# Performance work log

Hardware: AMD Instinct MI355X
Metric: run time of the kernel (lower is better)

## Reference

```python
import jax, jax.numpy as jnp
import numpy as np

INV_GRID_SCALING = 1.0 / 1.48
LRELU_SLOPE = 0.2  # LReLULayer = Linear + leaky_relu(0.2)

N_GRIDS = 64
N_FEATS = 2
GRID_RES = 64
NODES = 128
N_OUT = 1
N_PTS = 1048576


def trilinear_sample(grid, coords):
    """torch.nn.functional.grid_sample, 3D bilinear (trilinear), align_corners=True,
    padding_mode='zeros'. grid: [C, D, H, W]; coords: [N, 3] normalized (x,y,z) in [-1,1]
    where x indexes W, y indexes H, z indexes D. Returns [C, N]."""
    C, D, H, W = grid.shape
    fx = (coords[:, 0] + 1.0) * 0.5 * (W - 1)
    fy = (coords[:, 1] + 1.0) * 0.5 * (H - 1)
    fz = (coords[:, 2] + 1.0) * 0.5 * (D - 1)
    x0 = jnp.floor(fx); y0 = jnp.floor(fy); z0 = jnp.floor(fz)
    wx = fx - x0; wy = fy - y0; wz = fz - z0
    x0 = x0.astype(jnp.int32); y0 = y0.astype(jnp.int32); z0 = z0.astype(jnp.int32)
    x1 = x0 + 1; y1 = y0 + 1; z1 = z0 + 1

    def gather(zi, yi, xi):
        valid = ((zi >= 0) & (zi < D) & (yi >= 0) & (yi < H) & (xi >= 0) & (xi < W))
        zc = jnp.clip(zi, 0, D - 1)
        yc = jnp.clip(yi, 0, H - 1)
        xc = jnp.clip(xi, 0, W - 1)
        return grid[:, zc, yc, xc] * valid.astype(grid.dtype)[None, :]  # [C, N]

    c000 = gather(z0, y0, x0); c001 = gather(z0, y0, x1)
    c010 = gather(z0, y1, x0); c011 = gather(z0, y1, x1)
    c100 = gather(z1, y0, x0); c101 = gather(z1, y0, x1)
    c110 = gather(z1, y1, x0); c111 = gather(z1, y1, x1)

    c00 = c000 * (1 - wx) + c001 * wx
    c01 = c010 * (1 - wx) + c011 * wx
    c10 = c100 * (1 - wx) + c101 * wx
    c11 = c110 * (1 - wx) + c111 * wx
    c0 = c00 * (1 - wy) + c01 * wy
    c1 = c10 * (1 - wy) + c11 * wy
    return c0 * (1 - wz) + c1 * wz  # [C, N]


def amgsrn_forward(x, grid_scales, grid_translations, feature_grids,
                   W0, b0, W1, b1, W2, b2):
    G, C = feature_grids.shape[0], feature_grids.shape[1]
    N = x.shape[0]
    # Per-grid affine transform: [G, N, 3]
    coords = (x[None, :, :] * grid_scales[:, None, :]
              + grid_translations[:, None, :]) * INV_GRID_SCALING
    coords = jax.lax.stop_gradient(coords)  # torch detaches grid_sample coords
    # Multi-grid trilinear lookup: [G, C, N]
    feats = jax.vmap(trilinear_sample)(feature_grids, coords)
    # flatten(0,1).permute(1,0) -> [N, G*C]
    feats = feats.reshape(G * C, N).T
    # Decoder: LReLU(128) -> LReLU(128) -> Linear(1)
    h = jax.nn.leaky_relu(feats @ W0.T + b0, LRELU_SLOPE)
    h = jax.nn.leaky_relu(h @ W1.T + b1, LRELU_SLOPE)
    return h @ W2.T + b2


def setup_inputs() -> dict:
    key = jax.random.key(0)
    ks = jax.random.split(key, 10)
    x = jax.random.uniform(ks[0], (N_PTS, 3), jnp.float32, -1.0, 1.0)
    grid_scales = jax.random.uniform(ks[1], (N_GRIDS, 3), jnp.float32, 1.0, 1.25) * 1.48
    grid_translations = jax.random.uniform(ks[2], (N_GRIDS, 3), jnp.float32, -1.0, 1.0) * (grid_scales - 1.0)
    feature_grids = jax.random.uniform(ks[3], (N_GRIDS, N_FEATS, GRID_RES, GRID_RES, GRID_RES),
                                       jnp.float32, -1e-4, 1e-4)
    d_in = N_GRIDS * N_FEATS
    W0 = jax.random.normal(ks[4], (NODES, d_in), jnp.float32) * (2.0 / (d_in + NODES)) ** 0.5
    b0 = jax.random.normal(ks[5], (NODES,), jnp.float32) * 0.001
    W1 = jax.random.normal(ks[6], (NODES, NODES), jnp.float32) * (2.0 / (2 * NODES)) ** 0.5
    b1 = jax.random.normal(ks[7], (NODES,), jnp.float32) * 0.001
    W2 = jax.random.normal(ks[8], (N_OUT, NODES), jnp.float32) * (2.0 / (NODES + N_OUT)) ** 0.5
    b2 = jax.random.normal(ks[9], (N_OUT,), jnp.float32) * 0.001
    return {"x": x, "grid_scales": grid_scales, "grid_translations": grid_translations,
            "feature_grids": feature_grids, "W0": W0, "b0": b0,
            "W1": W1, "b1": b1, "W2": W2, "b2": b2}


def reference(x, grid_scales, grid_translations, feature_grids, W0, b0, W1, b1, W2, b2):
    return amgsrn_forward(x, grid_scales, grid_translations, feature_grids,
                          W0, b0, W1, b1, W2, b2)
```

## Files before the change

### kernel.cpp

```cpp
#include <hip/hip_runtime.h>

#define NG 64
#define RES 64
#define RES3 (RES*RES*RES)
#define NODES 128
#define NBINS 262144
#define FBLOCK 512
#define LDS_PITCH 132

#define PDIM 67
#define PZSTR 4489
#define PGSTR 300763
#define PFOLD 4557

typedef short    short8 __attribute__((ext_vector_type(8)));
typedef float    f32x16 __attribute__((ext_vector_type(16)));
typedef float    f32x4  __attribute__((ext_vector_type(4)));
typedef unsigned uint4v __attribute__((ext_vector_type(4)));

__device__ __forceinline__ float lrelu(float v) { return fmaxf(v, 0.2f * v); }

__device__ __forceinline__ unsigned cvtpk(float lo, float hi) {
    unsigned r;
    asm("v_cvt_pk_bf16_f32 %0, %1, %2" : "=v"(r) : "v"(lo), "v"(hi));
    return r;
}
__device__ __forceinline__ float lo16f(unsigned u) { return __uint_as_float(u << 16); }
__device__ __forceinline__ float hi16f(unsigned u) { return __uint_as_float(u & 0xffff0000u); }

__device__ __forceinline__ void swap32(unsigned &x, unsigned &y) {
    auto rr = __builtin_amdgcn_permlane32_swap(x, y, false, false);
    x = rr[0]; y = rr[1];
}

__device__ __forceinline__ int bin_of(float x, float y, float z) {
    int bx = min(max((int)((x + 1.0f) * 32.0f), 0), 63);
    int by = min(max((int)((y + 1.0f) * 32.0f), 0), 63);
    int bz = min(max((int)((z + 1.0f) * 32.0f), 0), 63);
    return (bz << 12) | (by << 6) | bx;
}

__device__ __forceinline__ int xcd_swz(int bid, int nblocks) {
    const int q = nblocks >> 3, r = nblocks & 7;
    const int xcd = bid & 7, idx = bid >> 3;
    return (xcd < r ? xcd * (q + 1) : r * (q + 1) + (xcd - r) * q) + idx;
}

__global__ void hist_k(const float* __restrict__ xs, unsigned* __restrict__ cnt, int npts) {
    int n = blockIdx.x * blockDim.x + threadIdx.x;
    if (n >= npts) return;
    atomicAdd(&cnt[bin_of(xs[n*3], xs[n*3+1], xs[n*3+2])], 1u);
}

__global__ void scan1_k(const unsigned* __restrict__ cnt, unsigned* __restrict__ offs,
                        unsigned* __restrict__ bsum) {
    __shared__ unsigned wsum[4];
    const int t = threadIdx.x, lane = t & 63, wid = t >> 6;
    const int base = blockIdx.x * 1024 + t * 4;
    const uint4v v = *(const uint4v*)(cnt + base);
    const unsigned run = v.x + v.y + v.z + v.w;
    unsigned inc = run;
    #pragma unroll
    for (int d = 1; d < 64; d <<= 1) {
        const unsigned u = __shfl_up(inc, d);
        if (lane >= d) inc += u;
    }
    if (lane == 63) wsum[wid] = inc;
    __syncthreads();
    unsigned wbase = 0;
    #pragma unroll
    for (int i = 0; i < 4; ++i) wbase += (i < wid) ? wsum[i] : 0u;
    const unsigned pre = wbase + inc - run;
    uint4v o;
    o.x = pre; o.y = o.x + v.x; o.z = o.y + v.y; o.w = o.z + v.z;
    *(uint4v*)(offs + base) = o;
    if (t == 255) bsum[blockIdx.x] = wbase + inc;
}

__global__ void scan2_k(const unsigned* __restrict__ bsum, unsigned* __restrict__ bbase) {
    __shared__ unsigned wsum[4];
    const int t = threadIdx.x, lane = t & 63, wid = t >> 6;
    const unsigned v = bsum[t];
    unsigned inc = v;
    #pragma unroll
    for (int d = 1; d < 64; d <<= 1) {
        const unsigned u = __shfl_up(inc, d);
        if (lane >= d) inc += u;
    }
    if (lane == 63) wsum[wid] = inc;
    __syncthreads();
    unsigned wbase = 0;
    #pragma unroll
    for (int i = 0; i < 4; ++i) wbase += (i < wid) ? wsum[i] : 0u;
    bbase[t] = wbase + inc - v;
}

__global__ void scan3_k(unsigned* __restrict__ offs, const unsigned* __restrict__ bbase) {
    const unsigned add = bbase[blockIdx.x];
    uint4v* o4 = (uint4v*)(offs) + blockIdx.x * 256 + threadIdx.x;
    uint4v v = *o4;
    v.x += add; v.y += add; v.z += add; v.w += add;
    *o4 = v;
}

__global__ void scatter_k(const float* __restrict__ xs, unsigned* __restrict__ offs,
                          float4* __restrict__ sp, int npts) {
    int n = blockIdx.x * blockDim.x + threadIdx.x;
    if (n >= npts) return;
    float x = xs[n*3], y = xs[n*3+1], z = xs[n*3+2];
    unsigned p = atomicAdd(&offs[bin_of(x, y, z)], 1u);
    sp[p] = make_float4(x, y, z, __int_as_float(n));
}

__global__ __launch_bounds__(256, 8)
void repack_pad_k(const float* __restrict__ g, float2* __restrict__ wg) {
    const int gz = blockIdx.x;
    const int gi = gz / PDIM;
    const int zp = gz - gi * PDIM;
    const float* base = g + ((size_t)gi << 19);
    float2* dst = wg + (size_t)gi * PGSTR + (size_t)zp * PZSTR;
    const int zr = zp - 1;
    const bool zok = (unsigned)zr < 64u;
    const int w    = threadIdx.x >> 6;
    const int lane = threadIdx.x & 63;
    for (int yp = w; yp < PDIM; yp += 4) {
        const int yr = yp - 1;
        const bool rowok = zok && (unsigned)yr < 64u;
        float2 v = make_float2(0.0f, 0.0f);
        if (rowok) {
            const int o = (zr * 64 + yr) * 64 + lane;
            v.x = base[o]; v.y = base[o + RES3];
        }
        float2* drow = dst + yp * PDIM;
        drow[1 + lane] = v;
        if (lane < 3) drow[lane == 0 ? 0 : 64 + lane] = make_float2(0.0f, 0.0f);
    }
}

__global__ void packw_k(const float* __restrict__ W0, const float* __restrict__ W1,
                        const float* __restrict__ b0, const float* __restrict__ b1,
                        const float* __restrict__ W2,
                        const float* __restrict__ scales, const float* __restrict__ trans,
                        unsigned* __restrict__ wp0, unsigned* __restrict__ wp1,
                        float* __restrict__ b0p, float* __restrict__ b1p, float* __restrict__ w2p,
                        float4* __restrict__ coefA, float4* __restrict__ coefB)
{
    const int i = blockIdx.x * 256 + threadIdx.x;
    if (i < 8192) {
        const int q = i & 3, l = (i >> 2) & 63, s = (i >> 8) & 7, jt = i >> 11;
        const int j  = jt * 32 + (l & 31);
        const int k0 = s * 16 + (l >> 5) * 8 + q * 2;
        wp0[i] = cvtpk(W0[j*128 + k0], W0[j*128 + k0 + 1]);
        wp1[i] = cvtpk(W1[j*128 + k0], W1[j*128 + k0 + 1]);
    } else if (i < 8320) {
        const int t = i - 8192;
        const int r = t & 15, h = (t >> 4) & 1, jt = t >> 5;
        const int f = 32*jt + (r & 3) + 8*(r >> 2) + 4*h;
        b0p[t] = b0[f]; b1p[t] = b1[f]; w2p[t] = W2[f];
    } else if (i < 8384) {
        const int g = i - 8320;
        constexpr float K = 31.5f / 1.48f;
        coefA[g] = make_float4(scales[g*3+0]*K, scales[g*3+1]*K, scales[g*3+2]*K, 0.0f);
        coefB[g] = make_float4(fmaf(trans[g*3+0], K, 31.5f),
                               fmaf(trans[g*3+1], K, 31.5f),
                               fmaf(trans[g*3+2], K, 31.5f), 0.0f);
    }
}

__global__ __launch_bounds__(256, 8)
void gather_k(const float4* __restrict__ sp,
              const float2* __restrict__ gpad,
              const float4* __restrict__ coefA,
              const float4* __restrict__ coefB,
              uint4v* __restrict__ feats4,
              int npts, int npad, int nblocks)
{
    const int bid  = xcd_swz(blockIdx.x, nblocks);
    const int sidx = bid * 256 + threadIdx.x;
    const float4 P = sp[min(sidx, npts - 1)];
    const float px = P.x, py = P.y, pz = P.z;
    const char* gb = (const char*)gpad;

    #pragma unroll 2
    for (int g4 = 0; g4 < 16; ++g4) {
        unsigned fw[4];
        #pragma unroll
        for (int q = 0; q < 4; ++q) {
            const int g = g4 * 4 + q;
            const float4 cA = coefA[g];
            const float4 cB = coefB[g];
            float fx = fmaf(px, cA.x, cB.x);
            float fy = fmaf(py, cA.y, cB.y);
            float fz = fmaf(pz, cA.z, cB.z);
            fx = fminf(fmaxf(fx, -1.0f), 64.0f);
            fy = fminf(fmaxf(fy, -1.0f), 64.0f);
            fz = fminf(fmaxf(fz, -1.0f), 64.0f);
            const float fx0 = floorf(fx), fy0 = floorf(fy), fz0 = floorf(fz);
            const float wx = fx - fx0, wy = fy - fy0, wz = fz - fz0;
            const int x0 = (int)fx0, y0 = (int)fy0, z0 = (int)fz0;

            const int cell = g * PGSTR + z0 * PZSTR + y0 * PDIM + x0 + PFOLD;
            const char* p = gb + (unsigned)cell * 8u;
            const f32x4 A00 = *(const f32x4*)(p);
            const f32x4 A01 = *(const f32x4*)(p + (unsigned)(PDIM*8));
            const f32x4 A10 = *(const f32x4*)(p + (unsigned)(PZSTR*8));
            const f32x4 A11 = *(const f32x4*)(p + (unsigned)((PZSTR+PDIM)*8));

            const float wx0 = 1.0f - wx, wy0 = 1.0f - wy, wz0 = 1.0f - wz;
            const float w00 = wz0*wy0, w01 = wz0*wy, w10 = wz*wy0, w11 = wz*wy;

            const float f0 = w00*fmaf(wx, A00.z, wx0*A00.x)
                           + w01*fmaf(wx, A01.z, wx0*A01.x)
                           + w10*fmaf(wx, A10.z, wx0*A10.x)
                           + w11*fmaf(wx, A11.z, wx0*A11.x);
            const float f1 = w00*fmaf(wx, A00.w, wx0*A00.y)
                           + w01*fmaf(wx, A01.w, wx0*A01.y)
                           + w10*fmaf(wx, A10.w, wx0*A10.y)
                           + w11*fmaf(wx, A11.w, wx0*A11.y);
            fw[q] = cvtpk(f0, f1);
        }
        __builtin_nontemporal_store((uint4v){fw[0], fw[1], fw[2], fw[3]},
                                    &feats4[(size_t)g4 * npad + sidx]);
    }
}

__global__ __launch_bounds__(512, 4)
void mlp_k(const float4* __restrict__ sp,
           const uint4v* __restrict__ feats4,
           const uint4v* __restrict__ wp0,
           const uint4v* __restrict__ wp1,
           const float*  __restrict__ b0p,
           const float*  __restrict__ b1p,
           const float*  __restrict__ w2p,
           const float*  __restrict__ b2,
           float* __restrict__ out, int npts, int npad)
{
    __shared__ uint4v sW0[2048];
    __shared__ uint4v sW1[2048];

    const int tid = threadIdx.x;
    #pragma unroll
    for (int i = 0; i < 4; ++i) {
        sW0[tid + 512*i] = wp0[tid + 512*i];
        sW1[tid + 512*i] = wp1[tid + 512*i];
    }

    const int w   = tid >> 6;
    const int l   = tid & 63;
    const int p31 = l & 31;
    const int h   = l >> 5;

    const int pidx = blockIdx.x * 256 + w * 32 + p31;

    f32x16 acc[4];
    #pragma unroll
    for (int jt = 0; jt < 4; ++jt)
        #pragma unroll
        for (int q4 = 0; q4 < 4; ++q4) {
            const float4 bv = *reinterpret_cast<const float4*>(b0p + jt*32 + h*16 + q4*4);
            acc[jt][q4*4+0] = bv.x; acc[jt][q4*4+1] = bv.y;
            acc[jt][q4*4+2] = bv.z; acc[jt][q4*4+3] = bv.w;
        }

    __syncthreads();

    #pragma unroll
    for (int s = 0; s < 8; ++s) {
        const uint4v fw = __builtin_nontemporal_load(&feats4[(size_t)(2*s + h) * npad + pidx]);
        const short8 bfr = __builtin_bit_cast(short8, fw);
        #pragma unroll
        for (int jt = 0; jt < 4; ++jt) {
            const short8 wa = __builtin_bit_cast(short8, sW0[(jt*8 + s)*64 + l]);
            acc[jt] = __builtin_amdgcn_mfma_f32_32x32x16_bf16(wa, bfr, acc[jt], 0, 0, 0);
        }
    }

    float psum = 0.0f;
    #pragma unroll
    for (int jt2 = 0; jt2 < 4; ++jt2) {
        f32x16 a2;
        #pragma unroll
        for (int q4 = 0; q4 < 4; ++q4) {
            const float4 bv = *reinterpret_cast<const float4*>(b1p + jt2*32 + h*16 + q4*4);
            a2[q4*4+0] = bv.x; a2[q4*4+1] = bv.y;
            a2[q4*4+2] = bv.z; a2[q4*4+3] = bv.w;
        }
        #pragma unroll
        for (int s = 0; s < 8; ++s) {
            const int jt    = s >> 1;
            const int rbase = (s & 1) * 4;
            unsigned hw[4], rw[4];
            #pragma unroll
            for (int i = 0; i < 4; ++i) {
                const int rp = rbase + i;
                float v0 = acc[jt][2*rp],  v1 = acc[jt][2*rp+1];
                v0 = fmaxf(v0, 0.2f*v0);   v1 = fmaxf(v1, 0.2f*v1);
                hw[i] = cvtpk(v0, v1);
                rw[i] = cvtpk(v0 - lo16f(hw[i]), v1 - hi16f(hw[i]));
            }
            swap32(hw[0], hw[2]); swap32(hw[1], hw[3]);
            swap32(rw[0], rw[2]); swap32(rw[1], rw[3]);

            const short8 wa = __builtin_bit_cast(short8, sW1[(jt2*8 + s)*64 + l]);
            const short8 bh = __builtin_bit_cast(short8, (uint4v){hw[0], hw[1], hw[2], hw[3]});
            const short8 br = __builtin_bit_cast(short8, (uint4v){rw[0], rw[1], rw[2], rw[3]});
            a2 = __builtin_amdgcn_mfma_f32_32x32x16_bf16(wa, bh, a2, 0, 0, 0);
            a2 = __builtin_amdgcn_mfma_f32_32x32x16_bf16(wa, br, a2, 0, 0, 0);
        }
        #pragma unroll
        for (int q4 = 0; q4 < 4; ++q4) {
            const float4 wv = *reinterpret_cast<const float4*>(w2p + jt2*32 + h*16 + q4*4);
            const float* wc = (const float*)&wv;
            #pragma unroll
            for (int c = 0; c < 4; ++c) {
                float h1 = a2[q4*4+c];
                h1 = fmaxf(h1, 0.2f*h1);
                psum = fmaf(h1, wc[c], psum);
            }
        }
    }
    const float tot = psum + __shfl_xor(psum, 32);
    if (h == 0 && pidx < npts) {
        const float ow = ((const float*)sp)[4*pidx + 3];
        out[__float_as_int(ow)] = tot + b2[0];
    }
}

__global__ __launch_bounds__(256, 3)
void fused_k(const float4* __restrict__ sp,
             const float2* __restrict__ gpad,
             const float4* __restrict__ coefA,
             const float4* __restrict__ coefB,
             const uint4v* __restrict__ wp0,
             const uint4v* __restrict__ wp1,
             const float*  __restrict__ b0p,
             const float*  __restrict__ b1p,
             const float*  __restrict__ w2p,
             const float*  __restrict__ b2,
             float* __restrict__ out, int npts, int nblocks)
{
    const int bid = xcd_swz(blockIdx.x, nblocks);
    const int tid = threadIdx.x;
    const int w   = tid >> 6;
    const int l   = tid & 63;
    const int p31 = l & 31;
    const int h   = l >> 5;
    const int h4  = h * 4;

    const int pidx = bid * 128 + w * 32 + p31;
    const float4 P = sp[min(pidx, npts - 1)];
    const float px = P.x, py = P.y, pz = P.z;

    f32x16 acc[4];
    #pragma unroll
    for (int jt = 0; jt < 4; ++jt)
        #pragma unroll
        for (int q4 = 0; q4 < 4; ++q4) {
            const float4 bv = *reinterpret_cast<const float4*>(b0p + jt*32 + h*16 + q4*4);
            acc[jt][q4*4+0] = bv.x; acc[jt][q4*4+1] = bv.y;
            acc[jt][q4*4+2] = bv.z; acc[jt][q4*4+3] = bv.w;
        }

    const char* gb = (const char*)gpad;

    #pragma unroll 1
    for (int s = 0; s < 8; ++s) {
        unsigned fr[4];
        #pragma unroll
        for (int gi = 0; gi < 4; ++gi) {
            const int g = s*8 + h4 + gi;
            const float4 cA = coefA[g];
            const float4 cB = coefB[g];
            float fx = fmaf(px, cA.x, cB.x);
            float fy = fmaf(py, cA.y, cB.y);
            float fz = fmaf(pz, cA.z, cB.z);
            fx = fminf(fmaxf(fx, -1.0f), 64.0f);
            fy = fminf(fmaxf(fy, -1.0f), 64.0f);
            fz = fminf(fmaxf(fz, -1.0f), 64.0f);
            const float fx0 = floorf(fx), fy0 = floorf(fy), fz0 = floorf(fz);
            const float wx = fx - fx0, wy = fy - fy0, wz = fz - fz0;
            const int x0 = (int)fx0, y0 = (int)fy0, z0 = (int)fz0;
            const int cell = g * PGSTR + z0 * PZSTR + y0 * PDIM + x0 + PFOLD;
            const char* p = gb + (unsigned)cell * 8u;
            const f32x4 A00 = *(const f32x4*)(p);
            const f32x4 A01 = *(const f32x4*)(p + (unsigned)(PDIM*8));
            const f32x4 A10 = *(const f32x4*)(p + (unsigned)(PZSTR*8));
            const f32x4 A11 = *(const f32x4*)(p + (unsigned)((PZSTR+PDIM)*8));
            const float wx0 = 1.0f - wx, wy0 = 1.0f - wy, wz0 = 1.0f - wz;
            const float w00 = wz0*wy0, w01 = wz0*wy, w10 = wz*wy0, w11 = wz*wy;
            const float f0 = w00*fmaf(wx, A00.z, wx0*A00.x)
                           + w01*fmaf(wx, A01.z, wx0*A01.x)
                           + w10*fmaf(wx, A10.z, wx0*A10.x)
                           + w11*fmaf(wx, A11.z, wx0*A11.x);
            const float f1 = w00*fmaf(wx, A00.w, wx0*A00.y)
                           + w01*fmaf(wx, A01.w, wx0*A01.y)
                           + w10*fmaf(wx, A10.w, wx0*A10.y)
                           + w11*fmaf(wx, A11.w, wx0*A11.y);
            fr[gi] = cvtpk(f0, f1);
        }
        const short8 bfr = __builtin_bit_cast(short8, (uint4v){fr[0], fr[1], fr[2], fr[3]});
        #pragma unroll
        for (int jt = 0; jt < 4; ++jt) {
            const short8 wa = __builtin_bit_cast(short8, wp0[(jt*8 + s)*64 + l]);
            acc[jt] = __builtin_amdgcn_mfma_f32_32x32x16_bf16(wa, bfr, acc[jt], 0, 0, 0);
        }
    }

    unsigned pkh[32], pkr[32];
    #pragma unroll
    for (int jt = 0; jt < 4; ++jt)
        #pragma unroll
        for (int rp = 0; rp < 8; ++rp) {
            float v0 = acc[jt][2*rp],  v1 = acc[jt][2*rp+1];
            v0 = fmaxf(v0, 0.2f*v0);   v1 = fmaxf(v1, 0.2f*v1);
            const unsigned ph = cvtpk(v0, v1);
            pkh[jt*8 + rp] = ph;
            pkr[jt*8 + rp] = cvtpk(v0 - lo16f(ph), v1 - hi16f(ph));
        }
    #pragma unroll
    for (int s = 0; s < 8; ++s)
        #pragma unroll
        for (int i = 0; i < 2; ++i) {
            swap32(pkh[4*s + i], pkh[4*s + i + 2]);
            swap32(pkr[4*s + i], pkr[4*s + i + 2]);
        }

    float psum = 0.0f;
    #pragma unroll
    for (int jt2 = 0; jt2 < 4; ++jt2) {
        f32x16 a2;
        #pragma unroll
        for (int q4 = 0; q4 < 4; ++q4) {
            const float4 bv = *reinterpret_cast<const float4*>(b1p + jt2*32 + h*16 + q4*4);
            a2[q4*4+0] = bv.x; a2[q4*4+1] = bv.y;
            a2[q4*4+2] = bv.z; a2[q4*4+3] = bv.w;
        }
        #pragma unroll
        for (int s = 0; s < 8; ++s) {
            const short8 wa = __builtin_bit_cast(short8, wp1[(jt2*8 + s)*64 + l]);
            const short8 bh = __builtin_bit_cast(short8,
                (uint4v){pkh[4*s], pkh[4*s+1], pkh[4*s+2], pkh[4*s+3]});
            const short8 br = __builtin_bit_cast(short8,
                (uint4v){pkr[4*s], pkr[4*s+1], pkr[4*s+2], pkr[4*s+3]});
            a2 = __builtin_amdgcn_mfma_f32_32x32x16_bf16(wa, bh, a2, 0, 0, 0);
            a2 = __builtin_amdgcn_mfma_f32_32x32x16_bf16(wa, br, a2, 0, 0, 0);
        }
        #pragma unroll
        for (int q4 = 0; q4 < 4; ++q4) {
            const float4 wv = *reinterpret_cast<const float4*>(w2p + jt2*32 + h*16 + q4*4);
            const float* wc = (const float*)&wv;
            #pragma unroll
            for (int c = 0; c < 4; ++c) {
                float h1 = a2[q4*4+c];
                h1 = fmaxf(h1, 0.2f*h1);
                psum = fmaf(h1, wc[c], psum);
            }
        }
    }
    const float tot = psum + __shfl_xor(psum, 32);
    if (h == 0 && pidx < npts)
        out[__float_as_int(P.w)] = tot + b2[0];
}

__global__ __launch_bounds__(FBLOCK, 2)
void amgsrn_fused(const float* __restrict__ xs, const float* __restrict__ scales,
                  const float* __restrict__ trans, const float* __restrict__ grids,
                  const float* __restrict__ W0, const float* __restrict__ b0,
                  const float* __restrict__ W1, const float* __restrict__ b1,
                  const float* __restrict__ W2, const float* __restrict__ b2,
                  float* __restrict__ out, int npts)
{
    __shared__ float sW0T[NODES * LDS_PITCH];
    __shared__ float sW1 [NODES * LDS_PITCH];
    const int tid = threadIdx.x;
    for (int i = tid; i < NODES * NODES; i += FBLOCK) {
        const int j = i >> 7, k = i & 127;
        sW0T[k * LDS_PITCH + j] = W0[i];
        sW1 [j * LDS_PITCH + k] = W1[i];
    }
    __syncthreads();
    const int n = blockIdx.x * FBLOCK + tid;
    if (n >= npts) return;
    const float px = xs[n*3], py = xs[n*3+1], pz = xs[n*3+2];
    constexpr float INV_SCALE = 1.0f / 1.48f;
    float h[NODES];
    #pragma unroll
    for (int j = 0; j < NODES; ++j) h[j] = b0[j];
    for (int g = 0; g < NG; ++g) {
        const float cx = (px * scales[g*3+0] + trans[g*3+0]) * INV_SCALE;
        const float cy = (py * scales[g*3+1] + trans[g*3+1]) * INV_SCALE;
        const float cz = (pz * scales[g*3+2] + trans[g*3+2]) * INV_SCALE;
        const float fx = (cx + 1.0f) * 31.5f, fy = (cy + 1.0f) * 31.5f, fz = (cz + 1.0f) * 31.5f;
        const float fx0 = floorf(fx), fy0 = floorf(fy), fz0 = floorf(fz);
        const float wx = fx - fx0, wy = fy - fy0, wz = fz - fz0;
        const int x0 = (int)fx0, y0 = (int)fy0, z0 = (int)fz0;
        const int xb = min(max(x0, 0), RES - 2);
        const float wx0 = ((unsigned)x0 < (unsigned)RES) ? (1.0f - wx) : 0.0f;
        const float wx1 = ((unsigned)(x0+1) < (unsigned)RES) ? wx : 0.0f;
        const float wA = (x0 == xb ? wx0 : 0.0f) + (x0 + 1 == xb ? wx1 : 0.0f);
        const float wB = (x0 == xb + 1 ? wx0 : 0.0f) + (x0 == xb ? wx1 : 0.0f);
        const float wy0 = ((unsigned)y0 < (unsigned)RES) ? (1.0f - wy) : 0.0f;
        const float wy1 = ((unsigned)(y0+1) < (unsigned)RES) ? wy : 0.0f;
        const int yc0 = min(max(y0, 0), RES-1), yc1 = min(max(y0+1, 0), RES-1);
        const float wz0 = ((unsigned)z0 < (unsigned)RES) ? (1.0f - wz) : 0.0f;
        const float wz1 = ((unsigned)(z0+1) < (unsigned)RES) ? wz : 0.0f;
        const int zc0 = min(max(z0, 0), RES-1), zc1 = min(max(z0+1, 0), RES-1);
        const float w00 = wz0*wy0, w01 = wz0*wy1, w10 = wz1*wy0, w11 = wz1*wy1;
        const int o00 = (zc0*RES+yc0)*RES+xb, o01 = (zc0*RES+yc1)*RES+xb;
        const int o10 = (zc1*RES+yc0)*RES+xb, o11 = (zc1*RES+yc1)*RES+xb;
        const float* gp = grids + (size_t)g * (2*RES3);
        const float* gq = gp + RES3;
        float f0 = w00*fmaf(wB, gp[o00+1], wA*gp[o00]);
        f0 = fmaf(w01, fmaf(wB, gp[o01+1], wA*gp[o01]), f0);
        f0 = fmaf(w10, fmaf(wB, gp[o10+1], wA*gp[o10]), f0);
        f0 = fmaf(w11, fmaf(wB, gp[o11+1], wA*gp[o11]), f0);
        float f1 = w00*fmaf(wB, gq[o00+1], wA*gq[o00]);
        f1 = fmaf(w01, fmaf(wB, gq[o01+1], wA*gq[o01]), f1);
        f1 = fmaf(w10, fmaf(wB, gq[o10+1], wA*gq[o10]), f1);
        f1 = fmaf(w11, fmaf(wB, gq[o11+1], wA*gq[o11]), f1);
        const float4* rowA = reinterpret_cast<const float4*>(&sW0T[(2*g) * LDS_PITCH]);
        const float4* rowB = reinterpret_cast<const float4*>(&sW0T[(2*g+1) * LDS_PITCH]);
        #pragma unroll
        for (int q = 0; q < NODES/4; ++q) {
            const float4 wa = rowA[q], wb = rowB[q];
            h[4*q+0] = fmaf(f1, wb.x, fmaf(f0, wa.x, h[4*q+0]));
            h[4*q+1] = fmaf(f1, wb.y, fmaf(f0, wa.y, h[4*q+1]));
            h[4*q+2] = fmaf(f1, wb.z, fmaf(f0, wa.z, h[4*q+2]));
            h[4*q+3] = fmaf(f1, wb.w, fmaf(f0, wa.w, h[4*q+3]));
        }
    }
    #pragma unroll
    for (int j = 0; j < NODES; ++j) h[j] = lrelu(h[j]);
    float oacc = b2[0];
    for (int j = 0; j < NODES; ++j) {
        const float4* row = reinterpret_cast<const float4*>(&sW1[j * LDS_PITCH]);
        float a0 = b1[j], a1 = 0.0f, a2 = 0.0f, a3 = 0.0f;
        #pragma unroll
        for (int q = 0; q < NODES/4; ++q) {
            const float4 wv = row[q];
            a0 = fmaf(h[4*q+0], wv.x, a0);
            a1 = fmaf(h[4*q+1], wv.y, a1);
            a2 = fmaf(h[4*q+2], wv.z, a2);
            a3 = fmaf(h[4*q+3], wv.w, a3);
        }
        const float sv = lrelu((a0 + a1) + (a2 + a3));
        oacc = fmaf(sv, W2[j], oacc);
    }
    out[n] = oacc;
}

extern "C" void kernel_launch(void* const* d_in, const int* in_sizes, int n_in,
                              void* d_out, int out_size, void* d_ws, size_t ws_size,
                              hipStream_t stream) {
    const float* xs     = (const float*)d_in[0];
    const float* scales = (const float*)d_in[1];
    const float* trans  = (const float*)d_in[2];
    const float* grids  = (const float*)d_in[3];
    const float* W0     = (const float*)d_in[4];
    const float* b0     = (const float*)d_in[5];
    const float* W1     = (const float*)d_in[6];
    const float* b1     = (const float*)d_in[7];
    const float* W2     = (const float*)d_in[8];
    const float* b2     = (const float*)d_in[9];
    float* out = (float*)d_out;

    const int npts = in_sizes[0] / 3;
    const int npad = (npts + 255) & ~255;
    const int nb   = (npts + 255) / 256;

    auto al = [](size_t v) { return (v + 255) & ~(size_t)255; };
    size_t off = 0;
    const size_t spOff    = off; off += al((size_t)npad * 16);
    const size_t cntOff   = off; off += al((size_t)NBINS * 4);
    const size_t offsOff  = off; off += al((size_t)NBINS * 4);
    const size_t bsumOff  = off; off += al(256 * 4);
    const size_t bbaseOff = off; off += al(256 * 4);
    const size_t wp0Off   = off; off += al((size_t)8192 * 4);
    const size_t wp1Off   = off; off += al((size_t)8192 * 4);
    const size_t b0pOff   = off; off += al(128 * 4);
    const size_t b1pOff   = off; off += al(128 * 4);
    const size_t w2pOff   = off; off += al(128 * 4);
    const size_t cAOff    = off; off += al(64 * 16);
    const size_t cBOff    = off; off += al(64 * 16);
    const size_t gpadOff  = off; off += al((size_t)NG * PGSTR * 8);
    const size_t needFused = off;
    const size_t featsOff = off; off += al((size_t)NG * npad * 4);
    const size_t needSplit = off;

    if (ws_size < needFused) {
        const int fb = (npts + FBLOCK - 1) / FBLOCK;
        amgsrn_fused<<<fb, FBLOCK, 0, stream>>>(xs, scales, trans, grids,
                                                W0, b0, W1, b1, W2, b2, out, npts);
        return;
    }

    char* ws = (char*)d_ws;
    float4*   sp    = (float4*)(ws + spOff);
    unsigned* cnt   = (unsigned*)(ws + cntOff);
    unsigned* offs  = (unsigned*)(ws + offsOff);
    unsigned* bsum  = (unsigned*)(ws + bsumOff);
    unsigned* bbase = (unsigned*)(ws + bbaseOff);
    unsigned* wp0   = (unsigned*)(ws + wp0Off);
    unsigned* wp1   = (unsigned*)(ws + wp1Off);
    float*    b0p   = (float*)(ws + b0pOff);
    float*    b1p   = (float*)(ws + b1pOff);
    float*    w2p   = (float*)(ws + w2pOff);
    float4*   coefA = (float4*)(ws + cAOff);
    float4*   coefB = (float4*)(ws + cBOff);
    float2*   gpad  = (float2*)(ws + gpadOff);
    uint4v*   feats4 = (uint4v*)(ws + featsOff);

    hipMemsetAsync(cnt, 0, (size_t)NBINS * 4, stream);
    packw_k<<<33, 256, 0, stream>>>(W0, W1, b0, b1, W2, scales, trans,
                                    wp0, wp1, b0p, b1p, w2p, coefA, coefB);
    repack_pad_k<<<NG * PDIM, 256, 0, stream>>>(grids, gpad);
    hist_k<<<nb, 256, 0, stream>>>(xs, cnt, npts);
    scan1_k<<<256, 256, 0, stream>>>(cnt, offs, bsum);
    scan2_k<<<1, 256, 0, stream>>>(bsum, bbase);
    scan3_k<<<256, 256, 0, stream>>>(offs, bbase);
    scatter_k<<<nb, 256, 0, stream>>>(xs, offs, sp, npts);

    if (ws_size >= needSplit) {
        const int gblocks = npad / 256;
        gather_k<<<gblocks, 256, 0, stream>>>(sp, gpad, coefA, coefB, feats4,
                                              npts, npad, gblocks);
        mlp_k<<<npad / 256, 512, 0, stream>>>(sp, feats4, (const uint4v*)wp0,
                                              (const uint4v*)wp1, b0p, b1p, w2p,
                                              b2, out, npts, npad);
    } else {
        const int fblocks = npad / 128;
        fused_k<<<fblocks, 256, 0, stream>>>(sp, gpad, coefA, coefB,
                                             (const uint4v*)wp0, (const uint4v*)wp1,
                                             b0p, b1p, w2p, b2, out, npts, fblocks);
    }
}
```

Baseline: 503.5 us.

## Fuse trilinear gather into MLP kernel with LDS-staged weights

Replaces the split gather_k + mlp_k pipeline, which wrote bf16 features to a global intermediate buffer and read them back, with a single 512-thread kernel. Each wave now computes its trilinear features directly in MFMA operand layout and feeds them to the first layer, with W0/W1 staged in LDS. This removes the feature buffer's global write and read traffic and one launch. In exchange, gather memory latency now sits inside the MFMA kernel, and the larger register and LDS footprint may reduce the latency hiding that the standalone gather kernel had.

```diff
diff --git a/kernel.cpp b/kernel.cpp
--- a/kernel.cpp
+++ b/kernel.cpp
@@ -167,26 +167,59 @@
     }
 }
 
-__global__ __launch_bounds__(256, 8)
-void gather_k(const float4* __restrict__ sp,
+__global__ __launch_bounds__(512, 4)
+void fusedw_k(const float4* __restrict__ sp,
               const float2* __restrict__ gpad,
               const float4* __restrict__ coefA,
               const float4* __restrict__ coefB,
-              uint4v* __restrict__ feats4,
-              int npts, int npad, int nblocks)
+              const uint4v* __restrict__ wp0,
+              const uint4v* __restrict__ wp1,
+              const float*  __restrict__ b0p,
+              const float*  __restrict__ b1p,
+              const float*  __restrict__ w2p,
+              const float*  __restrict__ b2,
+              float* __restrict__ out, int npts, int nblocks)
 {
-    const int bid  = xcd_swz(blockIdx.x, nblocks);
-    const int sidx = bid * 256 + threadIdx.x;
-    const float4 P = sp[min(sidx, npts - 1)];
+    __shared__ uint4v sW0[2048];
+    __shared__ uint4v sW1[2048];
+
+    const int tid = threadIdx.x;
+    #pragma unroll
+    for (int i = 0; i < 4; ++i) {
+        sW0[tid + 512*i] = wp0[tid + 512*i];
+        sW1[tid + 512*i] = wp1[tid + 512*i];
+    }
+
+    const int bid = xcd_swz(blockIdx.x, nblocks);
+    const int w   = tid >> 6;
+    const int l   = tid & 63;
+    const int p31 = l & 31;
+    const int h   = l >> 5;
+    const int h4  = h * 4;
+
+    const int pidx = bid * 256 + w * 32 + p31;
+    const float4 P = sp[min(pidx, npts - 1)];
     const float px = P.x, py = P.y, pz = P.z;
+
+    f32x16 acc[4];
+    #pragma unroll
+    for (int jt = 0; jt < 4; ++jt)
+        #pragma unroll
+        for (int q4 = 0; q4 < 4; ++q4) {
+            const float4 bv = *reinterpret_cast<const float4*>(b0p + jt*32 + h*16 + q4*4);
+            acc[jt][q4*4+0] = bv.x; acc[jt][q4*4+1] = bv.y;
+            acc[jt][q4*4+2] = bv.z; acc[jt][q4*4+3] = bv.w;
+        }
+
     const char* gb = (const char*)gpad;
-
-    #pragma unroll 2
-    for (int g4 = 0; g4 < 16; ++g4) {
-        unsigned fw[4];
-        #pragma unroll
-        for (int q = 0; q < 4; ++q) {
-            const int g = g4 * 4 + q;
+    __syncthreads();
+
+    #pragma unroll 1
+    for (int s = 0; s < 8; ++s) {
+        unsigned fr[4];
+        #pragma unroll
+        for (int gi = 0; gi < 4; ++gi) {
+            const int g = s*8 + h4 + gi;
             const float4 cA = coefA[g];
             const float4 cB = coefB[g];
             float fx = fmaf(px, cA.x, cB.x);
@@ -217,57 +250,9 @@
                            + w01*fmaf(wx, A01.w, wx0*A01.y)
                            + w10*fmaf(wx, A10.w, wx0*A10.y)
                            + w11*fmaf(wx, A11.w, wx0*A11.y);
-            fw[q] = cvtpk(f0, f1);
-        }
-        __builtin_nontemporal_store((uint4v){fw[0], fw[1], fw[2], fw[3]},
-                                    &feats4[(size_t)g4 * npad + sidx]);
-    }
-}
-
-__global__ __launch_bounds__(512, 4)
-void mlp_k(const float4* __restrict__ sp,
-           const uint4v* __restrict__ feats4,
-           const uint4v* __restrict__ wp0,
-           const uint4v* __restrict__ wp1,
-           const float*  __restrict__ b0p,
-           const float*  __restrict__ b1p,
-           const float*  __restrict__ w2p,
-           const float*  __restrict__ b2,
-           float* __restrict__ out, int npts, int npad)
-{
-    __shared__ uint4v sW0[2048];
-    __shared__ uint4v sW1[2048];
-
-    const int tid = threadIdx.x;
-    #pragma unroll
-    for (int i = 0; i < 4; ++i) {
-        sW0[tid + 512*i] = wp0[tid + 512*i];
-        sW1[tid + 512*i] = wp1[tid + 512*i];
-    }
-
-    const int w   = tid >> 6;
-    const int l   = tid & 63;
-    const int p31 = l & 31;
-    const int h   = l >> 5;
-
-    const int pidx = blockIdx.x * 256 + w * 32 + p31;
-
-    f32x16 acc[4];
-    #pragma unroll
-    for (int jt = 0; jt < 4; ++jt)
-        #pragma unroll
-        for (int q4 = 0; q4 < 4; ++q4) {
-            const float4 bv = *reinterpret_cast<const float4*>(b0p + jt*32 + h*16 + q4*4);
-            acc[jt][q4*4+0] = bv.x; acc[jt][q4*4+1] = bv.y;
-            acc[jt][q4*4+2] = bv.z; acc[jt][q4*4+3] = bv.w;
-        }
-
-    __syncthreads();
-
-    #pragma unroll
-    for (int s = 0; s < 8; ++s) {
-        const uint4v fw = __builtin_nontemporal_load(&feats4[(size_t)(2*s + h) * npad + pidx]);
-        const short8 bfr = __builtin_bit_cast(short8, fw);
+            fr[gi] = cvtpk(f0, f1);
+        }
+        const short8 bfr = __builtin_bit_cast(short8, (uint4v){fr[0], fr[1], fr[2], fr[3]});
         #pragma unroll
         for (int jt = 0; jt < 4; ++jt) {
             const short8 wa = __builtin_bit_cast(short8, sW0[(jt*8 + s)*64 + l]);
@@ -304,144 +289,6 @@
             const short8 wa = __builtin_bit_cast(short8, sW1[(jt2*8 + s)*64 + l]);
             const short8 bh = __builtin_bit_cast(short8, (uint4v){hw[0], hw[1], hw[2], hw[3]});
             const short8 br = __builtin_bit_cast(short8, (uint4v){rw[0], rw[1], rw[2], rw[3]});
-            a2 = __builtin_amdgcn_mfma_f32_32x32x16_bf16(wa, bh, a2, 0, 0, 0);
-            a2 = __builtin_amdgcn_mfma_f32_32x32x16_bf16(wa, br, a2, 0, 0, 0);
-        }
-        #pragma unroll
-        for (int q4 = 0; q4 < 4; ++q4) {
-            const float4 wv = *reinterpret_cast<const float4*>(w2p + jt2*32 + h*16 + q4*4);
-            const float* wc = (const float*)&wv;
-            #pragma unroll
-            for (int c = 0; c < 4; ++c) {
-                float h1 = a2[q4*4+c];
-                h1 = fmaxf(h1, 0.2f*h1);
-                psum = fmaf(h1, wc[c], psum);
-            }
-        }
-    }
-    const float tot = psum + __shfl_xor(psum, 32);
-    if (h == 0 && pidx < npts) {
-        const float ow = ((const float*)sp)[4*pidx + 3];
-        out[__float_as_int(ow)] = tot + b2[0];
-    }
-}
-
-__global__ __launch_bounds__(256, 3)
-void fused_k(const float4* __restrict__ sp,
-             const float2* __restrict__ gpad,
-             const float4* __restrict__ coefA,
-             const float4* __restrict__ coefB,
-             const uint4v* __restrict__ wp0,
-             const uint4v* __restrict__ wp1,
-             const float*  __restrict__ b0p,
-             const float*  __restrict__ b1p,
-             const float*  __restrict__ w2p,
-             const float*  __restrict__ b2,
-             float* __restrict__ out, int npts, int nblocks)
-{
-    const int bid = xcd_swz(blockIdx.x, nblocks);
-    const int tid = threadIdx.x;
-    const int w   = tid >> 6;
-    const int l   = tid & 63;
-    const int p31 = l & 31;
-    const int h   = l >> 5;
-    const int h4  = h * 4;
-
-    const int pidx = bid * 128 + w * 32 + p31;
-    const float4 P = sp[min(pidx, npts - 1)];
-    const float px = P.x, py = P.y, pz = P.z;
-
-    f32x16 acc[4];
-    #pragma unroll
-    for (int jt = 0; jt < 4; ++jt)
-        #pragma unroll
-        for (int q4 = 0; q4 < 4; ++q4) {
-            const float4 bv = *reinterpret_cast<const float4*>(b0p + jt*32 + h*16 + q4*4);
-            acc[jt][q4*4+0] = bv.x; acc[jt][q4*4+1] = bv.y;
-            acc[jt][q4*4+2] = bv.z; acc[jt][q4*4+3] = bv.w;
-        }
-
-    const char* gb = (const char*)gpad;
-
-    #pragma unroll 1
-    for (int s = 0; s < 8; ++s) {
-        unsigned fr[4];
-        #pragma unroll
-        for (int gi = 0; gi < 4; ++gi) {
-            const int g = s*8 + h4 + gi;
-            const float4 cA = coefA[g];
-            const float4 cB = coefB[g];
-            float fx = fmaf(px, cA.x, cB.x);
-            float fy = fmaf(py, cA.y, cB.y);
-            float fz = fmaf(pz, cA.z, cB.z);
-            fx = fminf(fmaxf(fx, -1.0f), 64.0f);
-            fy = fminf(fmaxf(fy, -1.0f), 64.0f);
-            fz = fminf(fmaxf(fz, -1.0f), 64.0f);
-            const float fx0 = floorf(fx), fy0 = floorf(fy), fz0 = floorf(fz);
-            const float wx = fx - fx0, wy = fy - fy0, wz = fz - fz0;
-            const int x0 = (int)fx0, y0 = (int)fy0, z0 = (int)fz0;
-            const int cell = g * PGSTR + z0 * PZSTR + y0 * PDIM + x0 + PFOLD;
-            const char* p = gb + (unsigned)cell * 8u;
-            const f32x4 A00 = *(const f32x4*)(p);
-            const f32x4 A01 = *(const f32x4*)(p + (unsigned)(PDIM*8));
-            const f32x4 A10 = *(const f32x4*)(p + (unsigned)(PZSTR*8));
-            const f32x4 A11 = *(const f32x4*)(p + (unsigned)((PZSTR+PDIM)*8));
-            const float wx0 = 1.0f - wx, wy0 = 1.0f - wy, wz0 = 1.0f - wz;
-            const float w00 = wz0*wy0, w01 = wz0*wy, w10 = wz*wy0, w11 = wz*wy;
-            const float f0 = w00*fmaf(wx, A00.z, wx0*A00.x)
-                           + w01*fmaf(wx, A01.z, wx0*A01.x)
-                           + w10*fmaf(wx, A10.z, wx0*A10.x)
-                           + w11*fmaf(wx, A11.z, wx0*A11.x);
-            const float f1 = w00*fmaf(wx, A00.w, wx0*A00.y)
-                           + w01*fmaf(wx, A01.w, wx0*A01.y)
-                           + w10*fmaf(wx, A10.w, wx0*A10.y)
-                           + w11*fmaf(wx, A11.w, wx0*A11.y);
-            fr[gi] = cvtpk(f0, f1);
-        }
-        const short8 bfr = __builtin_bit_cast(short8, (uint4v){fr[0], fr[1], fr[2], fr[3]});
-        #pragma unroll
-        for (int jt = 0; jt < 4; ++jt) {
-            const short8 wa = __builtin_bit_cast(short8, wp0[(jt*8 + s)*64 + l]);
-            acc[jt] = __builtin_amdgcn_mfma_f32_32x32x16_bf16(wa, bfr, acc[jt], 0, 0, 0);
-        }
-    }
-
-    unsigned pkh[32], pkr[32];
-    #pragma unroll
-    for (int jt = 0; jt < 4; ++jt)
-        #pragma unroll
-        for (int rp = 0; rp < 8; ++rp) {
-            float v0 = acc[jt][2*rp],  v1 = acc[jt][2*rp+1];
-            v0 = fmaxf(v0, 0.2f*v0);   v1 = fmaxf(v1, 0.2f*v1);
-            const unsigned ph = cvtpk(v0, v1);
-            pkh[jt*8 + rp] = ph;
-            pkr[jt*8 + rp] = cvtpk(v0 - lo16f(ph), v1 - hi16f(ph));
-        }
-    #pragma unroll
-    for (int s = 0; s < 8; ++s)
-        #pragma unroll
-        for (int i = 0; i < 2; ++i) {
-            swap32(pkh[4*s + i], pkh[4*s + i + 2]);
-            swap32(pkr[4*s + i], pkr[4*s + i + 2]);
-        }
-
-    float psum = 0.0f;
-    #pragma unroll
-    for (int jt2 = 0; jt2 < 4; ++jt2) {
-        f32x16 a2;
-        #pragma unroll
-        for (int q4 = 0; q4 < 4; ++q4) {
-            const float4 bv = *reinterpret_cast<const float4*>(b1p + jt2*32 + h*16 + q4*4);
-            a2[q4*4+0] = bv.x; a2[q4*4+1] = bv.y;
-            a2[q4*4+2] = bv.z; a2[q4*4+3] = bv.w;
-        }
-        #pragma unroll
-        for (int s = 0; s < 8; ++s) {
-            const short8 wa = __builtin_bit_cast(short8, wp1[(jt2*8 + s)*64 + l]);
-            const short8 bh = __builtin_bit_cast(short8,
-                (uint4v){pkh[4*s], pkh[4*s+1], pkh[4*s+2], pkh[4*s+3]});
-            const short8 br = __builtin_bit_cast(short8,
-                (uint4v){pkr[4*s], pkr[4*s+1], pkr[4*s+2], pkr[4*s+3]});
             a2 = __builtin_amdgcn_mfma_f32_32x32x16_bf16(wa, bh, a2, 0, 0, 0);
             a2 = __builtin_amdgcn_mfma_f32_32x32x16_bf16(wa, br, a2, 0, 0, 0);
         }
@@ -584,8 +431,6 @@
     const size_t cBOff    = off; off += al(64 * 16);
     const size_t gpadOff  = off; off += al((size_t)NG * PGSTR * 8);
     const size_t needFused = off;
-    const size_t featsOff = off; off += al((size_t)NG * npad * 4);
-    const size_t needSplit = off;
 
     if (ws_size < needFused) {
         const int fb = (npts + FBLOCK - 1) / FBLOCK;
@@ -608,7 +453,6 @@
     float4*   coefA = (float4*)(ws + cAOff);
     float4*   coefB = (float4*)(ws + cBOff);
     float2*   gpad  = (float2*)(ws + gpadOff);
-    uint4v*   feats4 = (uint4v*)(ws + featsOff);
 
     hipMemsetAsync(cnt, 0, (size_t)NBINS * 4, stream);
     packw_k<<<33, 256, 0, stream>>>(W0, W1, b0, b1, W2, scales, trans,
@@ -620,17 +464,8 @@
     scan3_k<<<256, 256, 0, stream>>>(offs, bbase);
     scatter_k<<<nb, 256, 0, stream>>>(xs, offs, sp, npts);
 
-    if (ws_size >= needSplit) {
-        const int gblocks = npad / 256;
-        gather_k<<<gblocks, 256, 0, stream>>>(sp, gpad, coefA, coefB, feats4,
-                                              npts, npad, gblocks);
-        mlp_k<<<npad / 256, 512, 0, stream>>>(sp, feats4, (const uint4v*)wp0,
-                                              (const uint4v*)wp1, b0p, b1p, w2p,
-                                              b2, out, npts, npad);
-    } else {
-        const int fblocks = npad / 128;
-        fused_k<<<fblocks, 256, 0, stream>>>(sp, gpad, coefA, coefB,
-                                             (const uint4v*)wp0, (const uint4v*)wp1,
-                                             b0p, b1p, w2p, b2, out, npts, fblocks);
-    }
-}
+    const int fblocks = npad / 256;
+    fusedw_k<<<fblocks, 512, 0, stream>>>(sp, gpad, coefA, coefB,
+                                          (const uint4v*)wp0, (const uint4v*)wp1,
+                                          b0p, b1p, w2p, b2, out, npts, fblocks);
+}
```

Result: no change. 495.7 us, median of 2 (-1.5%).
